# Kernel tuning notes

Hardware: AMD Instinct MI355X
Metric: run time of the kernel (lower is better)

Reference implementation:

```python
import jax, jax.numpy as jnp
import numpy as np

B = 16384      # batch of protein embeddings
C = 128        # n_channels
F = 5000       # number of GO terms (functions)
E_CHILD = 15000  # parent->child edges (~3 children per term)


def setup_inputs() -> dict:
    key = jax.random.key(0)
    k_x, k_w, k_p, k_c = jax.random.split(key, 4)
    x = jax.random.normal(k_x, (B, C), dtype=jnp.float32)
    W = jax.random.normal(k_w, (C, F), dtype=jnp.float32) * 0.05
    b = jnp.zeros((F,), dtype=jnp.float32)
    # random GO DAG edges; every node also gets a self-edge so the max
    # aggregation covers {self} U children, exactly like the torch loop
    parents = jax.random.randint(k_p, (E_CHILD,), 0, F, dtype=jnp.int32)
    childs = jax.random.randint(k_c, (E_CHILD,), 0, F, dtype=jnp.int32)
    self_idx = jnp.arange(F, dtype=jnp.int32)
    edge_parent = jnp.concatenate([self_idx, parents])  # [20000]
    edge_child = jnp.concatenate([self_idx, childs])    # [20000]
    return {"x": x, "W": W, "b": b,
            "edge_parent": edge_parent, "edge_child": edge_child}


def reference(x, W, b, edge_parent, edge_child):
    # Fused version of the 5000 separate Linear(C,1)+Sigmoid heads
    probs = jax.nn.sigmoid(x @ W + b)          # [B, F]
    # Hierarchical max over {self} U children via segment-max on edge list
    vals = probs.T[edge_child]                  # [E, B]
    agg = jax.ops.segment_max(vals, edge_parent, num_segments=F)  # [F, B]
    return agg.T                                # [B, F]
```

## Files before the change

### kernel.cpp

```cpp
#include <hip/hip_runtime.h>
#include <hip/hip_bf16.h>

#define BDIM 16384
#define CDIM 128
#define FDIM 5000
#define EDIM 20000
#define ELLW 16
#define MAXOVF 20000
#define NT4  10

typedef __attribute__((ext_vector_type(8))) short short8;
typedef __attribute__((ext_vector_type(4))) float f32x4;
typedef __attribute__((ext_vector_type(2))) float f32x2;
typedef __attribute__((ext_vector_type(2))) int i32x2;
typedef __attribute__((ext_vector_type(8))) unsigned short upk8;
typedef __attribute__((ext_vector_type(4))) unsigned short upk4;
typedef __attribute__((ext_vector_type(2))) unsigned int u32x2;

__device__ __forceinline__ unsigned short f2bf(float f) {
    unsigned int u = __builtin_bit_cast(unsigned int, f);
    u = (u + 0x7fffu + ((u >> 16) & 1u)) >> 16;
    return (unsigned short)u;
}
__device__ __forceinline__ float bf2f(unsigned short s) {
    unsigned int u = ((unsigned int)s) << 16;
    return __builtin_bit_cast(float, u);
}
__device__ __forceinline__ unsigned short q2bf(unsigned int w, int k) {
    float f = (float)((w >> (8 * k)) & 0xFFu);
    return (unsigned short)(__builtin_bit_cast(unsigned int, f) >> 16);
}
__device__ __forceinline__ upk8 umax8(upk8 a, upk8 b) {
#if __has_builtin(__builtin_elementwise_max)
    return __builtin_elementwise_max(a, b);
#else
    upk8 r;
    #pragma unroll
    for (int j = 0; j < 8; ++j) r[j] = a[j] > b[j] ? a[j] : b[j];
    return r;
#endif
}
__device__ __forceinline__ void gll16(const unsigned short* g, unsigned short* l) {
    __builtin_amdgcn_global_load_lds(
        (const __attribute__((address_space(1))) void*)g,
        (__attribute__((address_space(3))) void*)l, 16, 0, 0);
}

__global__ __launch_bounds__(256) void prep1_kernel(
    const float* __restrict__ x, const float* __restrict__ W,
    unsigned short* __restrict__ xb, unsigned short* __restrict__ wt,
    unsigned short* __restrict__ ell, int* __restrict__ cur,
    int* __restrict__ ovf_cnt)
{
    __shared__ float lt[128][33];
    int bid = blockIdx.x, tid = threadIdx.x;
    if (bid < 1024) {
        size_t base = (size_t)bid * 2048 + (size_t)tid * 8;
        const f32x4* p = (const f32x4*)(x + base);
        f32x4 v0 = p[0], v1 = p[1];
        short8 o;
        o[0] = (short)f2bf(v0[0]); o[1] = (short)f2bf(v0[1]);
        o[2] = (short)f2bf(v0[2]); o[3] = (short)f2bf(v0[3]);
        o[4] = (short)f2bf(v1[0]); o[5] = (short)f2bf(v1[1]);
        o[6] = (short)f2bf(v1[2]); o[7] = (short)f2bf(v1[3]);
        *(short8*)(xb + base) = o;
    } else if (bid < 1181) {
        int f0 = (bid - 1024) * 32;
        int f_l = tid & 31, k0 = (tid >> 5) * 16;
        #pragma unroll
        for (int i = 0; i < 16; ++i) {
            int f = f0 + f_l;
            lt[k0 + i][f_l] = (f < FDIM) ? W[(size_t)(k0 + i) * FDIM + f] : 0.f;
        }
        __syncthreads();
        int f_l2 = tid >> 3, ks = (tid & 7) * 16;
        int f = f0 + f_l2;
        if (f < FDIM) {
            short8 o0, o1;
            #pragma unroll
            for (int j = 0; j < 8; ++j) o0[j] = (short)f2bf(lt[ks + j][f_l2]);
            #pragma unroll
            for (int j = 0; j < 8; ++j) o1[j] = (short)f2bf(lt[ks + 8 + j][f_l2]);
            *(short8*)(wt + (size_t)f * 128 + ks)     = o0;
            *(short8*)(wt + (size_t)f * 128 + ks + 8) = o1;
        }
    } else {
        int p = (bid - 1181) * 256 + tid;
        if (p < FDIM) {
            upk8 s;
            #pragma unroll
            for (int j = 0; j < 8; ++j) s[j] = (unsigned short)p;
            *(upk8*)(ell + (size_t)p * ELLW)     = s;
            *(upk8*)(ell + (size_t)p * ELLW + 8) = s;
            cur[p] = 1;
        }
        if (p == FDIM) *ovf_cnt = 0;
    }
}

__global__ __launch_bounds__(256) void prep2_kernel(
    const int* __restrict__ epar, const int* __restrict__ echild,
    int* __restrict__ cur, unsigned short* __restrict__ ell,
    int* __restrict__ ovf_cnt, int* __restrict__ ovf_pairs)
{
    int i = blockIdx.x * 256 + threadIdx.x;
    if (i < EDIM) {
        int p = epar[i], c = echild[i];
        if (p != c) {
            int pos = atomicAdd(&cur[p], 1);
            if (pos < ELLW) {
                ell[(size_t)p * ELLW + pos] = (unsigned short)c;
            } else {
                int j = atomicAdd(ovf_cnt, 1);
                if (j < MAXOVF) { ovf_pairs[2 * j] = p; ovf_pairs[2 * j + 1] = c; }
            }
        }
    }
}

__global__ __launch_bounds__(512, 4) void gemm8i4_kernel(
    const unsigned short* __restrict__ xb,
    const unsigned short* __restrict__ wt,
    const float* __restrict__ bias,
    unsigned char* __restrict__ probs8)
{
    __shared__ unsigned short lA[128 * 128];
    __shared__ unsigned short lB[128 * 128];

    int bid0 = blockIdx.x;
    int bid  = (bid0 & 7) * (128 * NT4 / 8) + (bid0 >> 3);
    int bm = bid / NT4, bq = bid % NT4;
    int tid = threadIdx.x;
    int lane = tid & 63, w = tid >> 6;
    int wm = w >> 2, wn = w & 3;
    int g = lane >> 4, lr = lane & 15;
    int lrow = lane >> 4;
    int lcol = (lane & 15) << 4;

    auto stageA = [&]() {
        #pragma unroll
        for (int it = 0; it < 4; ++it) {
            int ci = w * 4 + it;
            int row = ci * 4 + lrow;
            int sw = lcol ^ ((row & 7) << 4);
            gll16(xb + ((size_t)(bm * 128 + row) << 7) + (sw >> 1),
                  lA + ci * 512);
        }
    };
    auto stageB = [&](int bn) {
        #pragma unroll
        for (int it = 0; it < 4; ++it) {
            int ci = w * 4 + it;
            int row = ci * 4 + lrow;
            int sw = lcol ^ ((row & 7) << 4);
            gll16(wt + ((size_t)(bn * 128 + row) << 7) + (sw >> 1),
                  lB + ci * 512);
        }
    };
    auto compute = [&](f32x4 (&acc)[4][2]) {
        #pragma unroll
        for (int ks = 0; ks < 4; ++ks) {
            int cbk = ks * 64 + g * 16;
            short8 af[4], bf[2];
            #pragma unroll
            for (int mi = 0; mi < 4; ++mi) {
                int row = wm * 64 + mi * 16 + lr;
                af[mi] = *(const short8*)((const char*)lA + row * 256 + (cbk ^ ((row & 7) << 4)));
            }
            #pragma unroll
            for (int nj = 0; nj < 2; ++nj) {
                int row = wn * 32 + nj * 16 + lr;
                bf[nj] = *(const short8*)((const char*)lB + row * 256 + (cbk ^ ((row & 7) << 4)));
            }
            #pragma unroll
            for (int mi = 0; mi < 4; ++mi)
                #pragma unroll
                for (int nj = 0; nj < 2; ++nj)
                    acc[mi][nj] = __builtin_amdgcn_mfma_f32_16x16x32_bf16(
                        af[mi], bf[nj], acc[mi][nj], 0, 0, 0);
        }
    };
    auto epilogue = [&](int bn, f32x4 (&acc)[4][2]) {
        #pragma unroll
        for (int nj = 0; nj < 2; ++nj) {
            int f = bn * 128 + wn * 32 + nj * 16 + lr;
            bool ok = (f < FDIM);
            float bb = ok ? bias[f] : 0.f;
            #pragma unroll
            for (int mi = 0; mi < 4; ++mi) {
                unsigned int pk = 0;
                #pragma unroll
                for (int j = 0; j < 4; ++j) {
                    float z = acc[mi][nj][j] + bb;
                    float pr = 1.0f / (1.0f + __expf(-z));
                    unsigned int q = (unsigned int)(pr * 255.f + 0.5f);
                    pk |= q << (8 * j);
                }
                if (ok) {
                    int slab = bm * 16 + wm * 8 + mi * 2 + (g >> 1);
                    *(unsigned int*)(probs8 + ((size_t)slab * FDIM + f) * 8 + (g & 1) * 4) = pk;
                }
            }
        }
    };

    stageA();
    stageB(bq * 4);
    __syncthreads();

    f32x4 zero = {0.f, 0.f, 0.f, 0.f};
    for (int t = 0; t < 4; ++t) {
        f32x4 acc[4][2];
        #pragma unroll
        for (int mi = 0; mi < 4; ++mi) { acc[mi][0] = zero; acc[mi][1] = zero; }
        compute(acc);
        if (t < 3) {
            __syncthreads();
            stageB(bq * 4 + t + 1);
            epilogue(bq * 4 + t, acc);
            __syncthreads();
        } else {
            epilogue(bq * 4 + t, acc);
        }
    }
}

__global__ __launch_bounds__(1024) void segmax10_kernel(
    const unsigned char* __restrict__ probs8,
    const int* __restrict__ cur, const unsigned short* __restrict__ ell,
    const int* __restrict__ ovf_cnt, const int* __restrict__ ovf_pairs,
    float* __restrict__ out)
{
    __shared__ unsigned short l[FDIM * 8];
    int slab = blockIdx.x;
    int b0 = slab * 8;
    int tid = threadIdx.x;
    const unsigned char* src = probs8 + (size_t)slab * FDIM * 8;

    for (int c = tid; c < FDIM; c += 1024) {
        u32x2 v = *(const u32x2*)(src + (size_t)c * 8);
        upk8 o;
        #pragma unroll
        for (int k = 0; k < 4; ++k) {
            o[k]     = q2bf(v[0], k);
            o[4 + k] = q2bf(v[1], k);
        }
        *(upk8*)(l + (size_t)c * 8) = o;
    }
    __syncthreads();

    int novf = *ovf_cnt; if (novf > MAXOVF) novf = MAXOVF;

    for (int p0 = tid * 2; p0 < FDIM; p0 += 2048) {
        int p1 = p0 + 1;
        i32x2 dg = *(const i32x2*)(cur + p0);
        upk4 ea = *(const upk4*)(ell + (size_t)p0 * ELLW);
        upk4 eb = *(const upk4*)(ell + (size_t)p1 * ELLW);
        upk8 ma = *(const upk8*)(l + (size_t)ea[0] * 8);
        upk8 mb = *(const upk8*)(l + (size_t)eb[0] * 8);
        ma = umax8(ma, *(const upk8*)(l + (size_t)ea[1] * 8));
        mb = umax8(mb, *(const upk8*)(l + (size_t)eb[1] * 8));
        ma = umax8(ma, *(const upk8*)(l + (size_t)ea[2] * 8));
        mb = umax8(mb, *(const upk8*)(l + (size_t)eb[2] * 8));
        ma = umax8(ma, *(const upk8*)(l + (size_t)ea[3] * 8));
        mb = umax8(mb, *(const upk8*)(l + (size_t)eb[3] * 8));
        if (dg[0] > 4) {
            upk4 e = *(const upk4*)(ell + (size_t)p0 * ELLW + 4);
            ma = umax8(ma, *(const upk8*)(l + (size_t)e[0] * 8));
            ma = umax8(ma, *(const upk8*)(l + (size_t)e[1] * 8));
            ma = umax8(ma, *(const upk8*)(l + (size_t)e[2] * 8));
            ma = umax8(ma, *(const upk8*)(l + (size_t)e[3] * 8));
        }
        if (dg[1] > 4) {
            upk4 e = *(const upk4*)(ell + (size_t)p1 * ELLW + 4);
            mb = umax8(mb, *(const upk8*)(l + (size_t)e[0] * 8));
            mb = umax8(mb, *(const upk8*)(l + (size_t)e[1] * 8));
            mb = umax8(mb, *(const upk8*)(l + (size_t)e[2] * 8));
            mb = umax8(mb, *(const upk8*)(l + (size_t)e[3] * 8));
        }
        if (dg[0] > 8) {
            upk8 e = *(const upk8*)(ell + (size_t)p0 * ELLW + 8);
            #pragma unroll
            for (int j = 0; j < 8; ++j)
                ma = umax8(ma, *(const upk8*)(l + (size_t)e[j] * 8));
        }
        if (dg[1] > 8) {
            upk8 e = *(const upk8*)(ell + (size_t)p1 * ELLW + 8);
            #pragma unroll
            for (int j = 0; j < 8; ++j)
                mb = umax8(mb, *(const upk8*)(l + (size_t)e[j] * 8));
        }
        if (dg[0] > ELLW) {
            for (int i = 0; i < novf; ++i)
                if (ovf_pairs[2 * i] == p0)
                    ma = umax8(ma, *(const upk8*)(l + (size_t)ovf_pairs[2 * i + 1] * 8));
        }
        if (dg[1] > ELLW) {
            for (int i = 0; i < novf; ++i)
                if (ovf_pairs[2 * i] == p1)
                    mb = umax8(mb, *(const upk8*)(l + (size_t)ovf_pairs[2 * i + 1] * 8));
        }
        size_t o = (size_t)b0 * FDIM + p0;
        #pragma unroll
        for (int r = 0; r < 8; ++r) {
            f32x2 v2;
            v2[0] = bf2f(ma[r]) * (1.f / 255.f);
            v2[1] = bf2f(mb[r]) * (1.f / 255.f);
            __builtin_nontemporal_store(v2, (f32x2*)(out + o + (size_t)r * FDIM));
        }
    }
}

extern "C" void kernel_launch(void* const* d_in, const int* in_sizes, int n_in,
                              void* d_out, int out_size, void* d_ws, size_t ws_size,
                              hipStream_t stream)
{
    const float* x     = (const float*)d_in[0];
    const float* W     = (const float*)d_in[1];
    const float* bias  = (const float*)d_in[2];
    const int*   epar  = (const int*)d_in[3];
    const int*   echild= (const int*)d_in[4];
    float* out = (float*)d_out;

    char* ws = (char*)d_ws;
    size_t off = 0;
    auto alloc = [&](size_t bytes) { size_t o = off; off = (off + bytes + 255) & ~(size_t)255; return o; };
    size_t o_probs  = alloc((size_t)BDIM * FDIM);
    size_t o_xb     = alloc((size_t)BDIM * CDIM * 2);
    size_t o_wt     = alloc((size_t)FDIM * CDIM * 2);
    size_t o_ell    = alloc((size_t)FDIM * ELLW * 2);
    size_t o_cur    = alloc((size_t)FDIM * 4);
    size_t o_ovfc   = alloc(4);
    size_t o_ovfp   = alloc((size_t)MAXOVF * 8);
    (void)ws_size; (void)in_sizes; (void)n_in; (void)out_size;

    unsigned char*  probs8 = (unsigned char*)(ws + o_probs);
    unsigned short* xb     = (unsigned short*)(ws + o_xb);
    unsigned short* wt     = (unsigned short*)(ws + o_wt);
    unsigned short* ell    = (unsigned short*)(ws + o_ell);
    int* cur      = (int*)(ws + o_cur);
    int* ovf_cnt  = (int*)(ws + o_ovfc);
    int* ovf_pairs= (int*)(ws + o_ovfp);

    prep1_kernel<<<1201, 256, 0, stream>>>(x, W, xb, wt, ell, cur, ovf_cnt);
    prep2_kernel<<<79, 256, 0, stream>>>(epar, echild, cur, ell, ovf_cnt, ovf_pairs);
    gemm8i4_kernel<<<128 * NT4, 512, 0, stream>>>(xb, wt, bias, probs8);
    segmax10_kernel<<<BDIM / 8, 1024, 0, stream>>>(probs8, cur, ell,
                                                   ovf_cnt, ovf_pairs, out);
}
```

Before: 179.0 us.

## Keep A fragments in registers, double-buffer B, widen segmax vector accesses

The GEMM now loads each warp's x fragments straight from global memory into registers once, instead of staging A through LDS. The freed LDS is used to double-buffer W tiles, so the next tile's load overlaps compute and one barrier per iteration goes away. The sigmoid uses a hardware reciprocal instead of a division. The segmax kernel handles four parents per thread, with 16-byte probability loads and 16-byte nontemporal output stores. The costs are higher register pressure from the af[4][4] array, which may reduce occupancy, and slightly less precise sigmoid values.

```diff
diff --git a/kernel.cpp b/kernel.cpp
--- a/kernel.cpp
+++ b/kernel.cpp
@@ -13,9 +13,11 @@
 typedef __attribute__((ext_vector_type(4))) float f32x4;
 typedef __attribute__((ext_vector_type(2))) float f32x2;
 typedef __attribute__((ext_vector_type(2))) int i32x2;
+typedef __attribute__((ext_vector_type(4))) int i32x4;
 typedef __attribute__((ext_vector_type(8))) unsigned short upk8;
 typedef __attribute__((ext_vector_type(4))) unsigned short upk4;
 typedef __attribute__((ext_vector_type(2))) unsigned int u32x2;
+typedef __attribute__((ext_vector_type(4))) unsigned int u32x4;
 
 __device__ __forceinline__ unsigned short f2bf(float f) {
     unsigned int u = __builtin_bit_cast(unsigned int, f);
@@ -38,6 +40,13 @@
     #pragma unroll
     for (int j = 0; j < 8; ++j) r[j] = a[j] > b[j] ? a[j] : b[j];
     return r;
+#endif
+}
+__device__ __forceinline__ float fast_rcp(float x) {
+#if __has_builtin(__builtin_amdgcn_rcpf)
+    return __builtin_amdgcn_rcpf(x);
+#else
+    return __frcp_rn(x);
 #endif
 }
 __device__ __forceinline__ void gll16(const unsigned short* g, unsigned short* l) {
@@ -118,14 +127,13 @@
     }
 }
 
-__global__ __launch_bounds__(512, 4) void gemm8i4_kernel(
+__global__ __launch_bounds__(512, 4) void gemm8r_kernel(
     const unsigned short* __restrict__ xb,
     const unsigned short* __restrict__ wt,
     const float* __restrict__ bias,
     unsigned char* __restrict__ probs8)
 {
-    __shared__ unsigned short lA[128 * 128];
-    __shared__ unsigned short lB[128 * 128];
+    __shared__ unsigned short lB[2][128 * 128];
 
     int bid0 = blockIdx.x;
     int bid  = (bid0 & 7) * (128 * NT4 / 8) + (bid0 >> 3);
@@ -137,49 +145,29 @@
     int lrow = lane >> 4;
     int lcol = (lane & 15) << 4;
 
-    auto stageA = [&]() {
-        #pragma unroll
-        for (int it = 0; it < 4; ++it) {
-            int ci = w * 4 + it;
-            int row = ci * 4 + lrow;
-            int sw = lcol ^ ((row & 7) << 4);
-            gll16(xb + ((size_t)(bm * 128 + row) << 7) + (sw >> 1),
-                  lA + ci * 512);
-        }
-    };
-    auto stageB = [&](int bn) {
+    auto stageB = [&](int bn, int buf) {
         #pragma unroll
         for (int it = 0; it < 4; ++it) {
             int ci = w * 4 + it;
             int row = ci * 4 + lrow;
             int sw = lcol ^ ((row & 7) << 4);
             gll16(wt + ((size_t)(bn * 128 + row) << 7) + (sw >> 1),
-                  lB + ci * 512);
+                  lB[buf] + ci * 512);
         }
     };
-    auto compute = [&](f32x4 (&acc)[4][2]) {
-        #pragma unroll
-        for (int ks = 0; ks < 4; ++ks) {
-            int cbk = ks * 64 + g * 16;
-            short8 af[4], bf[2];
-            #pragma unroll
-            for (int mi = 0; mi < 4; ++mi) {
-                int row = wm * 64 + mi * 16 + lr;
-                af[mi] = *(const short8*)((const char*)lA + row * 256 + (cbk ^ ((row & 7) << 4)));
-            }
-            #pragma unroll
-            for (int nj = 0; nj < 2; ++nj) {
-                int row = wn * 32 + nj * 16 + lr;
-                bf[nj] = *(const short8*)((const char*)lB + row * 256 + (cbk ^ ((row & 7) << 4)));
-            }
+
+    short8 af[4][4];
+    {
+        const unsigned short* xrow =
+            xb + ((size_t)(bm * 128 + wm * 64 + lr) << 7);
+        #pragma unroll
+        for (int ks = 0; ks < 4; ++ks)
             #pragma unroll
             for (int mi = 0; mi < 4; ++mi)
-                #pragma unroll
-                for (int nj = 0; nj < 2; ++nj)
-                    acc[mi][nj] = __builtin_amdgcn_mfma_f32_16x16x32_bf16(
-                        af[mi], bf[nj], acc[mi][nj], 0, 0, 0);
-        }
-    };
+                af[ks][mi] = *(const short8*)(xrow + (size_t)mi * 16 * 128
+                                              + ks * 32 + g * 8);
+    }
+
     auto epilogue = [&](int bn, f32x4 (&acc)[4][2]) {
         #pragma unroll
         for (int nj = 0; nj < 2; ++nj) {
@@ -192,7 +180,7 @@
                 #pragma unroll
                 for (int j = 0; j < 4; ++j) {
                     float z = acc[mi][nj][j] + bb;
-                    float pr = 1.0f / (1.0f + __expf(-z));
+                    float pr = fast_rcp(1.0f + __expf(-z));
                     unsigned int q = (unsigned int)(pr * 255.f + 0.5f);
                     pk |= q << (8 * j);
                 }
@@ -204,28 +192,41 @@
         }
     };
 
-    stageA();
-    stageB(bq * 4);
+    stageB(bq * 4, 0);
     __syncthreads();
 
     f32x4 zero = {0.f, 0.f, 0.f, 0.f};
+    #pragma unroll
     for (int t = 0; t < 4; ++t) {
         f32x4 acc[4][2];
         #pragma unroll
         for (int mi = 0; mi < 4; ++mi) { acc[mi][0] = zero; acc[mi][1] = zero; }
-        compute(acc);
-        if (t < 3) {
-            __syncthreads();
-            stageB(bq * 4 + t + 1);
-            epilogue(bq * 4 + t, acc);
-            __syncthreads();
-        } else {
-            epilogue(bq * 4 + t, acc);
-        }
-    }
-}
-
-__global__ __launch_bounds__(1024) void segmax10_kernel(
+
+        #pragma unroll
+        for (int ks = 0; ks < 4; ++ks) {
+            int cbk = ks * 64 + g * 16;
+            short8 bfr[2];
+            #pragma unroll
+            for (int nj = 0; nj < 2; ++nj) {
+                int row = wn * 32 + nj * 16 + lr;
+                bfr[nj] = *(const short8*)((const char*)lB[t & 1] + row * 256
+                                           + (cbk ^ ((row & 7) << 4)));
+            }
+            #pragma unroll
+            for (int mi = 0; mi < 4; ++mi)
+                #pragma unroll
+                for (int nj = 0; nj < 2; ++nj)
+                    acc[mi][nj] = __builtin_amdgcn_mfma_f32_16x16x32_bf16(
+                        af[ks][mi], bfr[nj], acc[mi][nj], 0, 0, 0);
+        }
+
+        if (t < 3) stageB(bq * 4 + t + 1, (t + 1) & 1);
+        epilogue(bq * 4 + t, acc);
+        if (t < 3) __syncthreads();
+    }
+}
+
+__global__ __launch_bounds__(1024) void segmax11_kernel(
     const unsigned char* __restrict__ probs8,
     const int* __restrict__ cur, const unsigned short* __restrict__ ell,
     const int* __restrict__ ovf_cnt, const int* __restrict__ ovf_pairs,
@@ -237,76 +238,61 @@
     int tid = threadIdx.x;
     const unsigned char* src = probs8 + (size_t)slab * FDIM * 8;
 
-    for (int c = tid; c < FDIM; c += 1024) {
-        u32x2 v = *(const u32x2*)(src + (size_t)c * 8);
-        upk8 o;
+    for (int c2 = tid; c2 < FDIM / 2; c2 += 1024) {
+        u32x4 v = *(const u32x4*)(src + (size_t)c2 * 16);
+        upk8 o0, o1;
         #pragma unroll
         for (int k = 0; k < 4; ++k) {
-            o[k]     = q2bf(v[0], k);
-            o[4 + k] = q2bf(v[1], k);
-        }
-        *(upk8*)(l + (size_t)c * 8) = o;
+            o0[k]     = q2bf(v[0], k);
+            o0[4 + k] = q2bf(v[1], k);
+            o1[k]     = q2bf(v[2], k);
+            o1[4 + k] = q2bf(v[3], k);
+        }
+        *(upk8*)(l + (size_t)c2 * 16)     = o0;
+        *(upk8*)(l + (size_t)c2 * 16 + 8) = o1;
     }
     __syncthreads();
 
     int novf = *ovf_cnt; if (novf > MAXOVF) novf = MAXOVF;
 
-    for (int p0 = tid * 2; p0 < FDIM; p0 += 2048) {
-        int p1 = p0 + 1;
-        i32x2 dg = *(const i32x2*)(cur + p0);
-        upk4 ea = *(const upk4*)(ell + (size_t)p0 * ELLW);
-        upk4 eb = *(const upk4*)(ell + (size_t)p1 * ELLW);
-        upk8 ma = *(const upk8*)(l + (size_t)ea[0] * 8);
-        upk8 mb = *(const upk8*)(l + (size_t)eb[0] * 8);
-        ma = umax8(ma, *(const upk8*)(l + (size_t)ea[1] * 8));
-        mb = umax8(mb, *(const upk8*)(l + (size_t)eb[1] * 8));
-        ma = umax8(ma, *(const upk8*)(l + (size_t)ea[2] * 8));
-        mb = umax8(mb, *(const upk8*)(l + (size_t)eb[2] * 8));
-        ma = umax8(ma, *(const upk8*)(l + (size_t)ea[3] * 8));
-        mb = umax8(mb, *(const upk8*)(l + (size_t)eb[3] * 8));
-        if (dg[0] > 4) {
-            upk4 e = *(const upk4*)(ell + (size_t)p0 * ELLW + 4);
-            ma = umax8(ma, *(const upk8*)(l + (size_t)e[0] * 8));
-            ma = umax8(ma, *(const upk8*)(l + (size_t)e[1] * 8));
-            ma = umax8(ma, *(const upk8*)(l + (size_t)e[2] * 8));
-            ma = umax8(ma, *(const upk8*)(l + (size_t)e[3] * 8));
-        }
-        if (dg[1] > 4) {
-            upk4 e = *(const upk4*)(ell + (size_t)p1 * ELLW + 4);
-            mb = umax8(mb, *(const upk8*)(l + (size_t)e[0] * 8));
-            mb = umax8(mb, *(const upk8*)(l + (size_t)e[1] * 8));
-            mb = umax8(mb, *(const upk8*)(l + (size_t)e[2] * 8));
-            mb = umax8(mb, *(const upk8*)(l + (size_t)e[3] * 8));
-        }
-        if (dg[0] > 8) {
-            upk8 e = *(const upk8*)(ell + (size_t)p0 * ELLW + 8);
-            #pragma unroll
-            for (int j = 0; j < 8; ++j)
-                ma = umax8(ma, *(const upk8*)(l + (size_t)e[j] * 8));
-        }
-        if (dg[1] > 8) {
-            upk8 e = *(const upk8*)(ell + (size_t)p1 * ELLW + 8);
-            #pragma unroll
-            for (int j = 0; j < 8; ++j)
-                mb = umax8(mb, *(const upk8*)(l + (size_t)e[j] * 8));
-        }
-        if (dg[0] > ELLW) {
-            for (int i = 0; i < novf; ++i)
-                if (ovf_pairs[2 * i] == p0)
-                    ma = umax8(ma, *(const upk8*)(l + (size_t)ovf_pairs[2 * i + 1] * 8));
-        }
-        if (dg[1] > ELLW) {
-            for (int i = 0; i < novf; ++i)
-                if (ovf_pairs[2 * i] == p1)
-                    mb = umax8(mb, *(const upk8*)(l + (size_t)ovf_pairs[2 * i + 1] * 8));
+    for (int p0 = tid * 4; p0 < FDIM; p0 += 4096) {
+        i32x4 dg = *(const i32x4*)(cur + p0);
+        upk8 m[4];
+        #pragma unroll
+        for (int j = 0; j < 4; ++j) {
+            int p = p0 + j;
+            upk4 ea = *(const upk4*)(ell + (size_t)p * ELLW);
+            m[j] = *(const upk8*)(l + (size_t)ea[0] * 8);
+            m[j] = umax8(m[j], *(const upk8*)(l + (size_t)ea[1] * 8));
+            m[j] = umax8(m[j], *(const upk8*)(l + (size_t)ea[2] * 8));
+            m[j] = umax8(m[j], *(const upk8*)(l + (size_t)ea[3] * 8));
+            if (dg[j] > 4) {
+                upk4 e = *(const upk4*)(ell + (size_t)p * ELLW + 4);
+                m[j] = umax8(m[j], *(const upk8*)(l + (size_t)e[0] * 8));
+                m[j] = umax8(m[j], *(const upk8*)(l + (size_t)e[1] * 8));
+                m[j] = umax8(m[j], *(const upk8*)(l + (size_t)e[2] * 8));
+                m[j] = umax8(m[j], *(const upk8*)(l + (size_t)e[3] * 8));
+            }
+            if (dg[j] > 8) {
+                upk8 e = *(const upk8*)(ell + (size_t)p * ELLW + 8);
+                #pragma unroll
+                for (int k = 0; k < 8; ++k)
+                    m[j] = umax8(m[j], *(const upk8*)(l + (size_t)e[k] * 8));
+            }
+            if (dg[j] > ELLW) {
+                for (int i = 0; i < novf; ++i)
+                    if (ovf_pairs[2 * i] == p)
+                        m[j] = umax8(m[j], *(const upk8*)(l + (size_t)ovf_pairs[2 * i + 1] * 8));
+            }
         }
         size_t o = (size_t)b0 * FDIM + p0;
         #pragma unroll
         for (int r = 0; r < 8; ++r) {
-            f32x2 v2;
-            v2[0] = bf2f(ma[r]) * (1.f / 255.f);
-            v2[1] = bf2f(mb[r]) * (1.f / 255.f);
-            __builtin_nontemporal_store(v2, (f32x2*)(out + o + (size_t)r * FDIM));
+            f32x4 v4;
+            #pragma unroll
+            for (int j = 0; j < 4; ++j)
+                v4[j] = bf2f(m[j][r]) * (1.f / 255.f);
+            __builtin_nontemporal_store(v4, (f32x4*)(out + o + (size_t)r * FDIM));
         }
     }
 }
@@ -344,7 +330,7 @@
 
     prep1_kernel<<<1201, 256, 0, stream>>>(x, W, xb, wt, ell, cur, ovf_cnt);
     prep2_kernel<<<79, 256, 0, stream>>>(epar, echild, cur, ell, ovf_cnt, ovf_pairs);
-    gemm8i4_kernel<<<128 * NT4, 512, 0, stream>>>(xb, wt, bias, probs8);
-    segmax10_kernel<<<BDIM / 8, 1024, 0, stream>>>(probs8, cur, ell,
+    gemm8r_kernel<<<128 * NT4, 512, 0, stream>>>(xb, wt, bias, probs8);
+    segmax11_kernel<<<BDIM / 8, 1024, 0, stream>>>(probs8, cur, ell,
                                                    ovf_cnt, ovf_pairs, out);
 }
```

After: 196.9 us. +10.0%, slower.
